# Performance work log

Hardware: AMD Instinct MI355X
Metric: run time of the kernel (lower is better)

## Reference

```python
import math
import jax, jax.numpy as jnp
import numpy as np

DIM = 3
NB = 8  # 2**DIM blades, grade-sorted: [1, e1, e2, e3, e12, e13, e23, e123]
GRADE_SLICES = [(0, 1), (1, 4), (4, 7), (7, 8)]
SUBSPACES = [1, 3, 3, 1]
GRADE_IDX = np.repeat(np.arange(4), SUBSPACES)  # blade -> grade index
EPS = 1e-6
SQRT2 = math.sqrt(2.0)


def _build_cayley():
    # Cl(3,0) Euclidean Cayley table, blades sorted by (grade, bitmask).
    masks = sorted(range(NB), key=lambda m: (bin(m).count("1"), m))
    pos = {m: i for i, m in enumerate(masks)}
    cay = np.zeros((NB, NB, NB), dtype=np.float32)
    for i, mi in enumerate(masks):
        for k, mk in enumerate(masks):
            a, s = mi >> 1, 0
            while a:
                s += bin(a & mk).count("1")
                a >>= 1
            cay[i, pos[mi ^ mk], k] = -1.0 if (s & 1) else 1.0
    triples = []
    for gi in range(4):
        for gj in range(4):
            for gk in range(4):
                (i0, i1), (j0, j1), (k0, k1) = GRADE_SLICES[gi], GRADE_SLICES[gj], GRADE_SLICES[gk]
                if np.any(cay[i0:i1, j0:j1, k0:k1] != 0):
                    triples.append((gi, gj, gk))
    return cay, triples

CAYLEY_NP, TRIPLES = _build_cayley()
NPATHS = len(TRIPLES)  # 20 nonzero grade-triple paths for Cl(3,0)


def mv_linear(x, w, b=None):
    # x: [B,n,8]; w: [m,n,4] (one weight per grade subspace); bias -> scalar blade only.
    w8 = w[..., GRADE_IDX]  # [m,n,8]
    out = jnp.einsum("bni,mni->bmi", x, w8)
    if b is not None:
        out = out.at[..., 0].add(b)
    return out


def grade_q(x):
    # per-grade squared magnitude (Euclidean metric -> all blade signs +1): [B,n,8]->[B,n,4]
    return jnp.stack([jnp.sum(x[..., s:e] ** 2, axis=-1) for s, e in GRADE_SLICES], axis=-1)


def normalization(x, a):
    # CGENN NormalizationLayer (init=0): interpolate per-grade norm toward 1 via sigmoid gate.
    norms = jnp.sqrt(grade_q(x))  # [B,n,4]
    sa = jax.nn.sigmoid(a)  # [n,4]
    norms = sa[None] * (norms - 1.0) + 1.0
    return x / (norms[..., GRADE_IDX] + EPS)


def mv_silu(x, a, b):
    # MVSiLU with invariant='mag2': gate on [scalar, q_grade1, q_grade2, q_grade3].
    q = grade_q(x)  # [B,n,4]
    inv = jnp.concatenate([x[..., :1], q[..., 1:]], axis=-1)  # [B,n,4]
    gate = a[None] * inv + b[None]
    return jax.nn.sigmoid(gate[..., GRADE_IDX]) * x


def fc_geometric_product(x, xr, w, cayley):
    # out[b,m,j] = sum_{n,i,k} x[b,n,i] * cayley[i,j,k] * W[m,n,path(gi,gj,gk)] * xr[b,n,k]
    B, n = x.shape[0], x.shape[1]
    m = w.shape[0]
    out = jnp.zeros((B, m, NB), dtype=x.dtype)
    for t, (gi, gj, gk) in enumerate(TRIPLES):
        (i0, i1), (j0, j1), (k0, k1) = GRADE_SLICES[gi], GRADE_SLICES[gj], GRADE_SLICES[gk]
        tmp = jnp.einsum("bni,ijk,bnk->bnj", x[..., i0:i1], cayley[i0:i1, j0:j1, k0:k1], xr[..., k0:k1])
        out = out.at[:, :, j0:j1].add(jnp.einsum("bnj,mn->bmj", tmp, w[:, :, t]))
    return out


def cw_geometric_product(x, xr, w, cayley):
    # channel-wise steerable GP: out[b,n,j] = sum_{i,k} x[b,n,i]*cayley[i,j,k]*w[n,path]*xr[b,n,k]
    out = jnp.zeros_like(x)
    for t, (gi, gj, gk) in enumerate(TRIPLES):
        (i0, i1), (j0, j1), (k0, k1) = GRADE_SLICES[gi], GRADE_SLICES[gj], GRADE_SLICES[gk]
        tmp = jnp.einsum("bni,ijk,bnk->bnj", x[..., i0:i1], cayley[i0:i1, j0:j1, k0:k1], xr[..., k0:k1])
        out = out.at[:, :, j0:j1].add(tmp * w[None, :, t, None])
    return out


B, IN, HID, OUT = 1024, 256, 512, 128


def setup_inputs():
    key = jax.random.key(0)
    ks = jax.random.split(key, 16)

    def nrm(k, shape, std):
        return jax.random.normal(k, shape, dtype=jnp.float32) * std

    s_in = 1.0 / math.sqrt(IN)
    s_hid = 1.0 / math.sqrt(HID)
    return {
        "x": jax.random.normal(ks[0], (B, IN, NB), dtype=jnp.float32),
        "lr1_w": nrm(ks[1], (IN, IN, 4), s_in),
        "n1_a": jnp.zeros((IN, 4), jnp.float32),
        "ll1_w": nrm(ks[2], (HID, IN, 4), s_in),
        "ll1_b": jnp.zeros((HID,), jnp.float32),
        "w1": nrm(ks[3], (HID, IN, NPATHS), 1.0 / math.sqrt(IN * (DIM + 1))),
        "act_a": jnp.ones((HID, 4), jnp.float32),
        "act_b": jnp.zeros((HID, 4), jnp.float32),
        "lrg_w": nrm(ks[4], (HID, HID, 4), s_hid),
        "ng_a": jnp.zeros((HID, 4), jnp.float32),
        "llg_w": nrm(ks[5], (HID, HID, 4), s_hid),
        "llg_b": jnp.zeros((HID,), jnp.float32),
        "wg": nrm(ks[6], (HID, NPATHS), 1.0 / math.sqrt(DIM + 1)),
        "lr2_w": nrm(ks[7], (HID, HID, 4), s_hid),
        "n2_a": jnp.zeros((HID, 4), jnp.float32),
        "ll2_w": nrm(ks[8], (OUT, HID, 4), s_hid),
        "ll2_b": jnp.zeros((OUT,), jnp.float32),
        "w2": nrm(ks[9], (OUT, HID, NPATHS), 1.0 / math.sqrt(HID * (DIM + 1))),
    }


def reference(x, lr1_w, n1_a, ll1_w, ll1_b, w1, act_a, act_b,
              lrg_w, ng_a, llg_w, llg_b, wg,
              lr2_w, n2_a, ll2_w, ll2_b, w2):
    cayley = jnp.asarray(CAYLEY_NP)
    # fcgp1: right linear -> normalize -> weighted geometric product + first-order term
    xr = normalization(mv_linear(x, lr1_w), n1_a)
    h = (mv_linear(x, ll1_w, ll1_b) + fc_geometric_product(x, xr, w1, cayley)) / SQRT2
    h = mv_silu(h, act_a, act_b)
    # channel-wise steerable geometric product layer
    hr = normalization(mv_linear(h, lrg_w), ng_a)
    h = (mv_linear(h, llg_w, llg_b) + cw_geometric_product(h, hr, wg, cayley)) / SQRT2
    h = mv_silu(h, act_a, act_b)
    # fcgp2
    hr = normalization(mv_linear(h, lr2_w), n2_a)
    out = (mv_linear(h, ll2_w, ll2_b) + fc_geometric_product(h, hr, w2, cayley)) / SQRT2
    return out
```

## Files before the change

kernel.cpp:

```cpp
#include <hip/hip_runtime.h>
#include <math.h>


typedef unsigned short u16;
typedef __attribute__((ext_vector_type(8))) short short8;
typedef __attribute__((ext_vector_type(4))) float f32x4;

#define RSQRT2F 0.70710678118654752440f

__device__ inline void gl_lds16(const void* g, void* l) {
  __builtin_amdgcn_global_load_lds(
      (const __attribute__((address_space(1))) void*)g,
      (__attribute__((address_space(3))) void*)l, 16, 0, 0);
}

__device__ constexpr int PP_I[64] = {
  0,0,0,0,0,0,0,0,  1,1,1,1,1,1,1,1,  2,2,2,2,2,2,2,2,  3,3,3,3,3,3,3,3,
  4,4,4,4,4,4,4,4,  5,5,5,5,5,5,5,5,  6,6,6,6,6,6,6,6,  7,7,7,7,7,7,7,7};
__device__ constexpr int PP_K[64] = {
  0,1,2,3,4,5,6,7,  0,1,2,3,4,5,6,7,  0,1,2,3,4,5,6,7,  0,1,2,3,4,5,6,7,
  0,1,2,3,4,5,6,7,  0,1,2,3,4,5,6,7,  0,1,2,3,4,5,6,7,  0,1,2,3,4,5,6,7};
__device__ constexpr int PP_C[64] = {
   0, 1, 2, 3, 4, 5, 6, 7,
   9, 8,15,16,13,14,21,20,
  10,15, 8,17,12,21,14,19,
  11,16,17, 8,21,12,13,18,
  29,24,23,35,22,34,33,28,
  30,25,35,23,34,22,32,27,
  31,35,25,24,33,32,22,26,
  43,42,41,40,39,38,37,36};
__device__ constexpr int PP_T[64] = {
   0, 1, 1, 1, 2, 2, 2, 3,
   5, 4, 7, 7, 6, 6, 9, 8,
   5, 7, 4, 7, 6, 9, 6, 8,
   5, 7, 7, 4, 9, 6, 6, 8,
  13,11,11,15,10,14,14,12,
  13,11,15,11,14,10,14,12,
  13,15,11,11,14,14,10,12,
  19,18,18,18,17,17,17,16};
__device__ constexpr int PP_J[64] = {
  0,1,2,3,4,5,6,7,
  1,0,4,5,2,3,7,6,
  2,4,0,6,1,7,3,5,
  3,5,6,0,7,1,2,4,
  4,2,1,7,0,6,5,3,
  5,3,7,1,6,0,4,2,
  6,7,3,2,5,4,0,1,
  7,6,5,4,3,2,1,0};
__device__ constexpr float PP_S[64] = {
  1, 1, 1, 1, 1, 1, 1, 1,
  1, 1, 1, 1, 1, 1, 1, 1,
  1,-1, 1, 1,-1,-1, 1,-1,
  1,-1,-1, 1, 1,-1,-1, 1,
  1,-1, 1, 1,-1,-1, 1,-1,
  1,-1,-1, 1, 1,-1,-1, 1,
  1, 1,-1, 1,-1, 1,-1,-1,
  1, 1,-1, 1,-1, 1,-1,-1};

__device__ constexpr int GJ_CNT[8] = {4,6,6,6,6,6,6,4};
__device__ constexpr int GJ_C[8][6] = {
  {0,8,22,36,0,0},
  {1,9,12,23,26,37},
  {2,10,13,24,27,38},
  {3,11,14,25,28,39},
  {4,15,18,29,32,40},
  {5,16,19,30,33,41},
  {6,17,20,31,34,42},
  {7,21,35,43,0,0}};
__device__ constexpr int GJ_T[8][6] = {
  {0,4,10,16,0,0},
  {1,5,6,11,12,17},
  {1,5,6,11,12,17},
  {1,5,6,11,12,17},
  {2,7,8,13,14,18},
  {2,7,8,13,14,18},
  {2,7,8,13,14,18},
  {3,9,15,19,0,0}};
__device__ constexpr int GRADE[8] = {0,1,1,1,2,2,2,3};

__device__ inline float sigm(float x) { return 1.0f / (1.0f + expf(-x)); }
__device__ inline u16 f2bf(float f) {
  unsigned u = __float_as_uint(f);
  return (u16)((u + 0x7fffu + ((u >> 16) & 1u)) >> 16);
}
__device__ inline float bf2f(u16 h) { return __uint_as_float(((unsigned)h) << 16); }

#define BT 128
#define MT 128
#define BKc 64

__global__ __launch_bounds__(256) void mfma_gemm(
    const u16* __restrict__ Alin, const u16* __restrict__ Pfeat,
    const u16* __restrict__ WLin, const u16* __restrict__ WLin2,
    const u16* __restrict__ WGp,
    float* __restrict__ out1, float* __restrict__ out2,
    int N, int M, int aug, int planeA, int planeO, int KSbits, int KCbits)
{
  const int zz    = blockIdx.z;
  const int set   = zz >> (3 + KSbits);
  const int rem   = zz & ((8 << KSbits) - 1);
  const int j     = rem >> KSbits;
  const int slice = rem & ((1 << KSbits) - 1);
  const u16* WL   = set ? WLin2 : WLin;
  float* outp     = set ? out2 : out1;

  const int b0   = blockIdx.y * BT;
  const int m0   = blockIdx.x * MT;
  const int tid  = threadIdx.x;
  const int lane = tid & 63;
  const int wave = tid >> 6;
  const int wr   = wave >> 1;
  const int wc   = wave & 1;
  const int l15  = lane & 15;
  const int lq   = lane >> 4;

  __shared__ u16 As[BT * BKc];
  __shared__ u16 Bs[MT * BKc];

  f32x4 zero = {0.f, 0.f, 0.f, 0.f};
  f32x4 acc[4][4];
  #pragma unroll
  for (int r = 0; r < 4; ++r)
    #pragma unroll
    for (int c = 0; c < 4; ++c) acc[r][c] = zero;

  const int g = GRADE[j];
  const int npass = aug ? (1 + GJ_CNT[j]) : 1;
  const int KC = 1 << KCbits;
  const int cper = (npass << KCbits) >> KSbits;
  const int cbeg = slice * cper;

  const int srow = lane >> 3;
  const int sslot = lane & 7;

  for (int ci = cbeg; ci < cbeg + cper; ++ci) {
    const int p  = ci >> KCbits;
    const int k0 = (ci & (KC - 1)) << 6;
    const u16* Abase = (p == 0) ? Alin + (size_t)j * planeA
                                : Pfeat + (size_t)GJ_C[j][p - 1] * planeA;
    const u16* Wbase = (p == 0) ? WL + (size_t)g * M * N
                                : WGp + (size_t)GJ_T[j][p - 1] * M * N;
    const u16* Asrc = Abase + (size_t)b0 * N + k0;
    const u16* Bsrc = Wbase + (size_t)m0 * N + k0;

    __syncthreads();
    #pragma unroll
    for (int q = 0; q < 4; ++q) {
      int inst = wave * 4 + q;
      int row  = inst * 8 + srow;
      int kg   = sslot ^ (row & 7);
      gl_lds16(Asrc + (size_t)row * N + kg * 8, &As[inst * 512]);
    }
    #pragma unroll
    for (int q = 0; q < 4; ++q) {
      int inst = wave * 4 + q;
      int row  = inst * 8 + srow;
      int kg   = sslot ^ (row & 7);
      gl_lds16(Bsrc + (size_t)row * N + kg * 8, &Bs[inst * 512]);
    }
    __syncthreads();

    #pragma unroll
    for (int s = 0; s < 2; ++s) {
      const int kq = s * 4 + lq;
      short8 af[4], bfr[4];
      #pragma unroll
      for (int r = 0; r < 4; ++r) {
        int row = wr * 64 + r * 16 + l15;
        af[r] = *(const short8*)(&As[row * BKc + (kq ^ (row & 7)) * 8]);
      }
      #pragma unroll
      for (int c = 0; c < 4; ++c) {
        int row = wc * 64 + c * 16 + l15;
        bfr[c] = *(const short8*)(&Bs[row * BKc + (kq ^ (row & 7)) * 8]);
      }
      #pragma unroll
      for (int r = 0; r < 4; ++r)
        #pragma unroll
        for (int c = 0; c < 4; ++c)
          acc[r][c] = __builtin_amdgcn_mfma_f32_16x16x32_bf16(af[r], bfr[c], acc[r][c], 0, 0, 0);
    }
  }

  float* obase = outp + (size_t)(slice * 8 + j) * planeO;
  #pragma unroll
  for (int r = 0; r < 4; ++r)
    #pragma unroll
    for (int c = 0; c < 4; ++c)
      #pragma unroll
      for (int e = 0; e < 4; ++e) {
        int bb = b0 + wr * 64 + r * 16 + lq * 4 + e;
        int mm = m0 + wc * 64 + c * 16 + l15;
        obase[(size_t)bb * M + mm] = acc[r][c][e];
      }
}

struct RepackDesc { const float* in; u16* out; int MN; int S; };
struct RepackArgs { RepackDesc d[8]; const float* x; u16* xp; int PS; };

__global__ void repack_all(RepackArgs a)
{
  int mn = blockIdx.x * 256 + threadIdx.x;
  if (blockIdx.y == 8) {
    if (mn >= a.PS) return;
    float v[8];
    *(float4*)(v)     = *(const float4*)(a.x + (size_t)mn * 8);
    *(float4*)(v + 4) = *(const float4*)(a.x + (size_t)mn * 8 + 4);
    #pragma unroll
    for (int jj = 0; jj < 8; ++jj) a.xp[(size_t)jj * a.PS + mn] = f2bf(v[jj]);
    return;
  }
  RepackDesc d = a.d[blockIdx.y];
  if (mn >= d.MN) return;
  if (d.S == 4) {
    float4 v = ((const float4*)d.in)[mn];
    d.out[(size_t)0 * d.MN + mn] = f2bf(v.x);
    d.out[(size_t)1 * d.MN + mn] = f2bf(v.y);
    d.out[(size_t)2 * d.MN + mn] = f2bf(v.z);
    d.out[(size_t)3 * d.MN + mn] = f2bf(v.w);
  } else {
    #pragma unroll
    for (int q = 0; q < 5; ++q) {
      float4 v = *(const float4*)(d.in + (size_t)mn * 20 + q * 4);
      d.out[(size_t)(q * 4 + 0) * d.MN + mn] = f2bf(v.x);
      d.out[(size_t)(q * 4 + 1) * d.MN + mn] = f2bf(v.y);
      d.out[(size_t)(q * 4 + 2) * d.MN + mn] = f2bf(v.z);
      d.out[(size_t)(q * 4 + 3) * d.MN + mn] = f2bf(v.w);
    }
  }
}

__global__ void pair_norm_p(const u16* __restrict__ up, const float* __restrict__ vpart,
                            const float* __restrict__ na, u16* __restrict__ Pp,
                            int PS, int M, int KS)
{
  int t = blockIdx.x * 256 + threadIdx.x;
  if (t >= PS) return;
  int m = t % M;
  float u[8], v[8];
  #pragma unroll
  for (int jj = 0; jj < 8; ++jj) {
    u[jj] = bf2f(up[(size_t)jj * PS + t]);
    float s = 0.f;
    for (int sl = 0; sl < KS; ++sl) s += vpart[(size_t)(sl * 8 + jj) * PS + t];
    v[jj] = s;
  }
  float q[4];
  q[0] = sqrtf(v[0] * v[0]);
  q[1] = sqrtf(v[1] * v[1] + v[2] * v[2] + v[3] * v[3]);
  q[2] = sqrtf(v[4] * v[4] + v[5] * v[5] + v[6] * v[6]);
  q[3] = sqrtf(v[7] * v[7]);
  float sc[4];
  #pragma unroll
  for (int gg = 0; gg < 4; ++gg) {
    float sa = sigm(na[m * 4 + gg]);
    sc[gg] = 1.0f / (sa * (q[gg] - 1.0f) + 1.0f + 1e-6f);
  }
  #pragma unroll
  for (int jj = 0; jj < 8; ++jj) v[jj] *= sc[GRADE[jj]];
  float p[44];
  #pragma unroll
  for (int c = 0; c < 44; ++c) p[c] = 0.f;
  #pragma unroll
  for (int e = 0; e < 64; ++e)
    p[PP_C[e]] += PP_S[e] * u[PP_I[e]] * v[PP_K[e]];
  #pragma unroll
  for (int c = 0; c < 44; ++c) Pp[(size_t)c * PS + t] = f2bf(p[c]);
}

__global__ void bias_silu_p(const float* __restrict__ hpart, const float* __restrict__ bias,
                            const float* __restrict__ ga, const float* __restrict__ gb,
                            u16* __restrict__ sh, int PS, int M, int KS)
{
  int t = blockIdx.x * 256 + threadIdx.x;
  if (t >= PS) return;
  int m = t % M;
  float v[8];
  #pragma unroll
  for (int jj = 0; jj < 8; ++jj) {
    float s = 0.f;
    for (int sl = 0; sl < KS; ++sl) s += hpart[(size_t)(sl * 8 + jj) * PS + t];
    v[jj] = s;
  }
  v[0] += bias[m];
  #pragma unroll
  for (int jj = 0; jj < 8; ++jj) v[jj] *= RSQRT2F;
  float inv[4];
  inv[0] = v[0];
  inv[1] = v[1]*v[1] + v[2]*v[2] + v[3]*v[3];
  inv[2] = v[4]*v[4] + v[5]*v[5] + v[6]*v[6];
  inv[3] = v[7]*v[7];
  float gt[4];
  #pragma unroll
  for (int gg = 0; gg < 4; ++gg)
    gt[gg] = sigm(ga[m * 4 + gg] * inv[gg] + gb[m * 4 + gg]);
  #pragma unroll
  for (int jj = 0; jj < 8; ++jj)
    sh[(size_t)jj * PS + t] = f2bf(v[jj] * gt[GRADE[jj]]);
}

__global__ void cw_silu_p(const float* __restrict__ llg, const u16* __restrict__ up,
                          const float* __restrict__ hrraw, const float* __restrict__ na,
                          const float* __restrict__ wg, const float* __restrict__ bias,
                          const float* __restrict__ ga, const float* __restrict__ gb,
                          u16* __restrict__ sh, int PS, int M)
{
  int t = blockIdx.x * 256 + threadIdx.x;
  if (t >= PS) return;
  int n = t % M;
  float acc[8], u[8], v[8], w[20];
  #pragma unroll
  for (int jj = 0; jj < 8; ++jj) {
    acc[jj] = llg[(size_t)jj * PS + t];
    u[jj]   = bf2f(up[(size_t)jj * PS + t]);
    v[jj]   = hrraw[(size_t)jj * PS + t];
  }
  float q[4];
  q[0] = sqrtf(v[0] * v[0]);
  q[1] = sqrtf(v[1] * v[1] + v[2] * v[2] + v[3] * v[3]);
  q[2] = sqrtf(v[4] * v[4] + v[5] * v[5] + v[6] * v[6]);
  q[3] = sqrtf(v[7] * v[7]);
  float sc[4];
  #pragma unroll
  for (int gg = 0; gg < 4; ++gg) {
    float sa = sigm(na[n * 4 + gg]);
    sc[gg] = 1.0f / (sa * (q[gg] - 1.0f) + 1.0f + 1e-6f);
  }
  #pragma unroll
  for (int jj = 0; jj < 8; ++jj) v[jj] *= sc[GRADE[jj]];
  #pragma unroll
  for (int qq = 0; qq < 5; ++qq)
    *(float4*)(w + qq * 4) = *(const float4*)(wg + (size_t)n * 20 + qq * 4);
  acc[0] += bias[n];
  #pragma unroll
  for (int e = 0; e < 64; ++e)
    acc[PP_J[e]] += PP_S[e] * u[PP_I[e]] * v[PP_K[e]] * w[PP_T[e]];
  #pragma unroll
  for (int jj = 0; jj < 8; ++jj) acc[jj] *= RSQRT2F;
  float inv[4];
  inv[0] = acc[0];
  inv[1] = acc[1]*acc[1] + acc[2]*acc[2] + acc[3]*acc[3];
  inv[2] = acc[4]*acc[4] + acc[5]*acc[5] + acc[6]*acc[6];
  inv[3] = acc[7]*acc[7];
  float gt[4];
  #pragma unroll
  for (int gg = 0; gg < 4; ++gg)
    gt[gg] = sigm(ga[n * 4 + gg] * inv[gg] + gb[n * 4 + gg]);
  #pragma unroll
  for (int jj = 0; jj < 8; ++jj)
    sh[(size_t)jj * PS + t] = f2bf(acc[jj] * gt[GRADE[jj]]);
}

__global__ void final_p(const float* __restrict__ pre, const float* __restrict__ bias,
                        float* __restrict__ outp, int PS, int M, int KS)
{
  int t = blockIdx.x * 256 + threadIdx.x;
  if (t >= PS) return;
  int m = t % M;
  float v[8];
  #pragma unroll
  for (int jj = 0; jj < 8; ++jj) {
    float s = 0.f;
    for (int sl = 0; sl < KS; ++sl) s += pre[(size_t)(sl * 8 + jj) * PS + t];
    v[jj] = s;
  }
  v[0] += bias[m];
  #pragma unroll
  for (int jj = 0; jj < 8; ++jj) v[jj] *= RSQRT2F;
  *(float4*)(outp + (size_t)t * 8)     = *(float4*)(v);
  *(float4*)(outp + (size_t)t * 8 + 4) = *(float4*)(v + 4);
}

extern "C" void kernel_launch(void* const* d_in, const int* in_sizes, int n_in,
                              void* d_out, int out_size, void* d_ws, size_t ws_size,
                              hipStream_t stream)
{
  const float* x     = (const float*)d_in[0];
  const float* lr1_w = (const float*)d_in[1];
  const float* n1_a  = (const float*)d_in[2];
  const float* ll1_w = (const float*)d_in[3];
  const float* ll1_b = (const float*)d_in[4];
  const float* w1    = (const float*)d_in[5];
  const float* act_a = (const float*)d_in[6];
  const float* act_b = (const float*)d_in[7];
  const float* lrg_w = (const float*)d_in[8];
  const float* ng_a  = (const float*)d_in[9];
  const float* llg_w = (const float*)d_in[10];
  const float* llg_b = (const float*)d_in[11];
  const float* wg    = (const float*)d_in[12];
  const float* lr2_w = (const float*)d_in[13];
  const float* n2_a  = (const float*)d_in[14];
  const float* ll2_w = (const float*)d_in[15];
  const float* ll2_b = (const float*)d_in[16];
  const float* w2    = (const float*)d_in[17];
  float* out = (float*)d_out;

  u16* W = (u16*)d_ws;
  size_t o = 0;
  u16* WL1  = W + o; o +=  262144;
  u16* WLL1 = W + o; o +=  524288;
  u16* WG1  = W + o; o += 2621440;
  u16* WLRG = W + o; o += 1048576;
  u16* WLLG = W + o; o += 1048576;
  u16* WLR2 = W + o; o += 1048576;
  u16* WLL2 = W + o; o +=  262144;
  u16* WG2  = W + o; o += 1310720;
  u16* XB   = W + o; o += 2097152;
  u16* HB   = W + o; o += 4194304;
  u16* P    = W + o; o += 23068672;
  float* f1 = (float*)(W + o);
  float* f2 = f1 + 8388608;
  float* hrP  = f2;
  float* llgP = f2 + 4194304;

  dim3 blk(256);
  const int PS1 = 1024 * 256, PS2 = 1024 * 512, PSO = 1024 * 128;

  RepackArgs ra = {{
    {lr1_w, WL1, 65536, 4}, {ll1_w, WLL1, 131072, 4}, {w1, WG1, 131072, 20},
    {lrg_w, WLRG, 262144, 4}, {llg_w, WLLG, 262144, 4}, {lr2_w, WLR2, 262144, 4},
    {ll2_w, WLL2, 65536, 4}, {w2, WG2, 65536, 20}},
    x, XB, PS1};
  repack_all<<<dim3(1024, 9), blk, 0, stream>>>(ra);

  mfma_gemm<<<dim3(2, 8, 16), blk, 0, stream>>>(XB, nullptr, WL1, nullptr, nullptr,
      f1, nullptr, 256, 256, 0, PS1, PS1, 1, 2);
  pair_norm_p<<<PS1 / 256, blk, 0, stream>>>(XB, f1, n1_a, P, PS1, 256, 2);
  mfma_gemm<<<dim3(4, 8, 16), blk, 0, stream>>>(XB, P, WLL1, nullptr, WG1,
      f1, nullptr, 256, 512, 1, PS1, PS2, 1, 2);
  bias_silu_p<<<PS2 / 256, blk, 0, stream>>>(f1, ll1_b, act_a, act_b, HB, PS2, 512, 2);

  mfma_gemm<<<dim3(4, 8, 16), blk, 0, stream>>>(HB, nullptr, WLRG, WLLG, nullptr,
      hrP, llgP, 512, 512, 0, PS2, PS2, 0, 3);
  cw_silu_p<<<PS2 / 256, blk, 0, stream>>>(llgP, HB, hrP, ng_a, wg, llg_b, act_a, act_b,
      HB, PS2, 512);

  mfma_gemm<<<dim3(4, 8, 16), blk, 0, stream>>>(HB, nullptr, WLR2, nullptr, nullptr,
      f1, nullptr, 512, 512, 0, PS2, PS2, 1, 3);
  pair_norm_p<<<PS2 / 256, blk, 0, stream>>>(HB, f1, n2_a, P, PS2, 512, 2);
  mfma_gemm<<<dim3(1, 8, 64), blk, 0, stream>>>(HB, P, WLL2, nullptr, WG2,
      f1, nullptr, 512, 128, 1, PS2, PSO, 3, 3);
  final_p<<<PSO / 256, blk, 0, stream>>>(f1, ll2_b, out, PSO, 128, 8);
}
```

Baseline: 261.8 us.

## Fuse all stages into one persistent kernel with grid barriers and bf16 intermediates

Replaces the ten separate launches with a single persistent 256-block kernel that loops over GEMM tiles and elementwise work and uses a software grid-wide atomic barrier between stages. GEMM LDS loads are double-buffered with explicit waitcnt so the next k-chunk loads overlap the current MFMAs. Most intermediate GEMM outputs are now stored in bf16 instead of fp32, and split-K is removed in several GEMMs. This cuts launch overhead and intermediate memory traffic. The costs are lower precision, fewer parallel tiles in some stages, and a grid barrier that hangs if not all 256 blocks are co-resident.

```diff
diff --git a/kernel.cpp b/kernel.cpp
--- a/kernel.cpp
+++ b/kernel.cpp
@@ -7,6 +7,10 @@
 typedef __attribute__((ext_vector_type(4))) float f32x4;
 
 #define RSQRT2F 0.70710678118654752440f
+#define NBLK 256
+#define PS1C (1024 * 256)
+#define PS2C (1024 * 512)
+#define PSOC (1024 * 128)
 
 __device__ inline void gl_lds16(const void* g, void* l) {
   __builtin_amdgcn_global_load_lds(
@@ -85,27 +89,83 @@
 }
 __device__ inline float bf2f(u16 h) { return __uint_as_float(((unsigned)h) << 16); }
 
-#define BT 128
-#define MT 128
-#define BKc 64
-
-__global__ __launch_bounds__(256) void mfma_gemm(
+__device__ void gsync(int* bar, int phase) {
+  __syncthreads();
+  if (threadIdx.x == 0) {
+    __threadfence();
+    if (__hip_atomic_fetch_add(&bar[0], 1, __ATOMIC_ACQ_REL,
+                               __HIP_MEMORY_SCOPE_AGENT) == NBLK - 1) {
+      __hip_atomic_store(&bar[0], 0, __ATOMIC_RELAXED, __HIP_MEMORY_SCOPE_AGENT);
+      __hip_atomic_store(&bar[1], phase, __ATOMIC_RELEASE, __HIP_MEMORY_SCOPE_AGENT);
+    } else {
+      while (__hip_atomic_load(&bar[1], __ATOMIC_ACQUIRE,
+                               __HIP_MEMORY_SCOPE_AGENT) < phase)
+        __builtin_amdgcn_s_sleep(8);
+    }
+    __threadfence();
+  }
+  __syncthreads();
+}
+
+struct KArgs {
+  const float* rin[8]; u16* rout[8]; int rMN[8]; int rS[8];
+  const float* x; u16* XB;
+  const float *n1_a, *ll1_b, *act_a, *act_b, *ng_a, *llg_b, *wg, *n2_a, *ll2_b;
+  u16 *WL1, *WLL1, *WG1, *WLRG, *WLLG, *WLR2, *WLL2, *WG2;
+  u16 *HB, *P, *PB16, *hr16, *llg16;
+  float* f1;
+  float* out;
+  int* bar;
+};
+
+__device__ void repack_stage(const KArgs& a) {
+  const int base = blockIdx.x * 256 + threadIdx.x;
+  #pragma unroll 1
+  for (int sec = 0; sec < 8; ++sec) {
+    const float* in = a.rin[sec];
+    u16* outp = a.rout[sec];
+    const int MN = a.rMN[sec];
+    if (a.rS[sec] == 4) {
+      for (int mn = base; mn < MN; mn += NBLK * 256) {
+        float4 v = ((const float4*)in)[mn];
+        outp[(size_t)0 * MN + mn] = f2bf(v.x);
+        outp[(size_t)1 * MN + mn] = f2bf(v.y);
+        outp[(size_t)2 * MN + mn] = f2bf(v.z);
+        outp[(size_t)3 * MN + mn] = f2bf(v.w);
+      }
+    } else {
+      for (int mn = base; mn < MN; mn += NBLK * 256) {
+        #pragma unroll
+        for (int q = 0; q < 5; ++q) {
+          float4 v = *(const float4*)(in + (size_t)mn * 20 + q * 4);
+          outp[(size_t)(q * 4 + 0) * MN + mn] = f2bf(v.x);
+          outp[(size_t)(q * 4 + 1) * MN + mn] = f2bf(v.y);
+          outp[(size_t)(q * 4 + 2) * MN + mn] = f2bf(v.z);
+          outp[(size_t)(q * 4 + 3) * MN + mn] = f2bf(v.w);
+        }
+      }
+    }
+  }
+  for (int mn = base; mn < PS1C; mn += NBLK * 256) {
+    float v[8];
+    *(float4*)(v)     = *(const float4*)(a.x + (size_t)mn * 8);
+    *(float4*)(v + 4) = *(const float4*)(a.x + (size_t)mn * 8 + 4);
+    #pragma unroll
+    for (int jj = 0; jj < 8; ++jj) a.XB[(size_t)jj * PS1C + mn] = f2bf(v[jj]);
+  }
+}
+
+__device__ void gemm_stage(
     const u16* __restrict__ Alin, const u16* __restrict__ Pfeat,
     const u16* __restrict__ WLin, const u16* __restrict__ WLin2,
     const u16* __restrict__ WGp,
-    float* __restrict__ out1, float* __restrict__ out2,
-    int N, int M, int aug, int planeA, int planeO, int KSbits, int KCbits)
+    void* __restrict__ out1, void* __restrict__ out2,
+    int N, int M, int aug, int planeA, int planeO,
+    int KSbits, int KCbits, int out16)
 {
-  const int zz    = blockIdx.z;
-  const int set   = zz >> (3 + KSbits);
-  const int rem   = zz & ((8 << KSbits) - 1);
-  const int j     = rem >> KSbits;
-  const int slice = rem & ((1 << KSbits) - 1);
-  const u16* WL   = set ? WLin2 : WLin;
-  float* outp     = set ? out2 : out1;
-
-  const int b0   = blockIdx.y * BT;
-  const int m0   = blockIdx.x * MT;
+  __shared__ u16 AsB[2][8192];
+  __shared__ u16 BsB[2][8192];
+
   const int tid  = threadIdx.x;
   const int lane = tid & 63;
   const int wave = tid >> 6;
@@ -113,262 +173,285 @@
   const int wc   = wave & 1;
   const int l15  = lane & 15;
   const int lq   = lane >> 4;
-
-  __shared__ u16 As[BT * BKc];
-  __shared__ u16 Bs[MT * BKc];
-
-  f32x4 zero = {0.f, 0.f, 0.f, 0.f};
-  f32x4 acc[4][4];
-  #pragma unroll
-  for (int r = 0; r < 4; ++r)
-    #pragma unroll
-    for (int c = 0; c < 4; ++c) acc[r][c] = zero;
-
-  const int g = GRADE[j];
-  const int npass = aug ? (1 + GJ_CNT[j]) : 1;
-  const int KC = 1 << KCbits;
-  const int cper = (npass << KCbits) >> KSbits;
-  const int cbeg = slice * cper;
-
-  const int srow = lane >> 3;
+  const int srow  = lane >> 3;
   const int sslot = lane & 7;
 
-  for (int ci = cbeg; ci < cbeg + cper; ++ci) {
-    const int p  = ci >> KCbits;
-    const int k0 = (ci & (KC - 1)) << 6;
-    const u16* Abase = (p == 0) ? Alin + (size_t)j * planeA
-                                : Pfeat + (size_t)GJ_C[j][p - 1] * planeA;
-    const u16* Wbase = (p == 0) ? WL + (size_t)g * M * N
-                                : WGp + (size_t)GJ_T[j][p - 1] * M * N;
-    const u16* Asrc = Abase + (size_t)b0 * N + k0;
-    const u16* Bsrc = Wbase + (size_t)m0 * N + k0;
-
-    __syncthreads();
-    #pragma unroll
-    for (int q = 0; q < 4; ++q) {
-      int inst = wave * 4 + q;
-      int row  = inst * 8 + srow;
-      int kg   = sslot ^ (row & 7);
-      gl_lds16(Asrc + (size_t)row * N + kg * 8, &As[inst * 512]);
-    }
-    #pragma unroll
-    for (int q = 0; q < 4; ++q) {
-      int inst = wave * 4 + q;
-      int row  = inst * 8 + srow;
-      int kg   = sslot ^ (row & 7);
-      gl_lds16(Bsrc + (size_t)row * N + kg * 8, &Bs[inst * 512]);
-    }
-    __syncthreads();
-
-    #pragma unroll
-    for (int s = 0; s < 2; ++s) {
-      const int kq = s * 4 + lq;
-      short8 af[4], bfr[4];
+  const int NMX = M >> 7;
+  const int nsets = WLin2 ? 2 : 1;
+  const int KS = 1 << KSbits, KC = 1 << KCbits;
+  const int ntiles = nsets * 8 * KS * 8 * NMX;
+
+  #pragma unroll 1
+  for (int t = blockIdx.x; t < ntiles; t += NBLK) {
+    int tmp = t;
+    const int mx = tmp % NMX; tmp /= NMX;
+    const int by = tmp & 7; tmp >>= 3;
+    const int slice = tmp & (KS - 1); tmp >>= KSbits;
+    const int j = tmp & 7;
+    const int set = tmp >> 3;
+    const u16* WL = set ? WLin2 : WLin;
+    void* outp = set ? out2 : out1;
+    const int b0 = by * 128, m0 = mx * 128;
+    const int g = GRADE[j];
+    const int npass = aug ? (1 + GJ_CNT[j]) : 1;
+    const int cper = (npass << KCbits) >> KSbits;
+    const int cbeg = slice * cper;
+
+    f32x4 acc[4][4];
+    #pragma unroll
+    for (int r = 0; r < 4; ++r)
       #pragma unroll
-      for (int r = 0; r < 4; ++r) {
-        int row = wr * 64 + r * 16 + l15;
-        af[r] = *(const short8*)(&As[row * BKc + (kq ^ (row & 7)) * 8]);
+      for (int c = 0; c < 4; ++c) acc[r][c] = {0.f, 0.f, 0.f, 0.f};
+
+    {
+      const int ci = cbeg;
+      const int p = ci >> KCbits, k0 = (ci & (KC - 1)) << 6;
+      const u16* Ab = (p == 0) ? Alin + (size_t)j * planeA
+                               : Pfeat + (size_t)GJ_C[j][p - 1] * planeA;
+      const u16* Wb = (p == 0) ? WL + (size_t)g * M * N
+                               : WGp + (size_t)GJ_T[j][p - 1] * (size_t)M * N;
+      const u16* As0 = Ab + (size_t)b0 * N + k0;
+      const u16* Bs0 = Wb + (size_t)m0 * N + k0;
+      #pragma unroll
+      for (int q = 0; q < 4; ++q) {
+        int inst = wave * 4 + q, row = inst * 8 + srow;
+        int kg = sslot ^ (row & 7);
+        gl_lds16(As0 + (size_t)row * N + kg * 8, &AsB[0][inst * 512]);
       }
       #pragma unroll
-      for (int c = 0; c < 4; ++c) {
-        int row = wc * 64 + c * 16 + l15;
-        bfr[c] = *(const short8*)(&Bs[row * BKc + (kq ^ (row & 7)) * 8]);
+      for (int q = 0; q < 4; ++q) {
+        int inst = wave * 4 + q, row = inst * 8 + srow;
+        int kg = sslot ^ (row & 7);
+        gl_lds16(Bs0 + (size_t)row * N + kg * 8, &BsB[0][inst * 512]);
       }
+    }
+
+    #pragma unroll 1
+    for (int ci = cbeg; ci < cbeg + cper; ++ci) {
+      const int buf = (ci - cbeg) & 1;
+      if (ci + 1 < cbeg + cper) {
+        const int cn = ci + 1;
+        const int p = cn >> KCbits, k0 = (cn & (KC - 1)) << 6;
+        const u16* Ab = (p == 0) ? Alin + (size_t)j * planeA
+                                 : Pfeat + (size_t)GJ_C[j][p - 1] * planeA;
+        const u16* Wb = (p == 0) ? WL + (size_t)g * M * N
+                                 : WGp + (size_t)GJ_T[j][p - 1] * (size_t)M * N;
+        const u16* As1 = Ab + (size_t)b0 * N + k0;
+        const u16* Bs1 = Wb + (size_t)m0 * N + k0;
+        #pragma unroll
+        for (int q = 0; q < 4; ++q) {
+          int inst = wave * 4 + q, row = inst * 8 + srow;
+          int kg = sslot ^ (row & 7);
+          gl_lds16(As1 + (size_t)row * N + kg * 8, &AsB[1 - buf][inst * 512]);
+        }
+        #pragma unroll
+        for (int q = 0; q < 4; ++q) {
+          int inst = wave * 4 + q, row = inst * 8 + srow;
+          int kg = sslot ^ (row & 7);
+          gl_lds16(Bs1 + (size_t)row * N + kg * 8, &BsB[1 - buf][inst * 512]);
+        }
+        asm volatile("s_waitcnt vmcnt(8)\n\ts_barrier" ::: "memory");
+      } else {
+        asm volatile("s_waitcnt vmcnt(0)\n\ts_barrier" ::: "memory");
+      }
+
+      const u16* As = &AsB[buf][0];
+      const u16* Bs = &BsB[buf][0];
       #pragma unroll
-      for (int r = 0; r < 4; ++r)
-        #pragma unroll
-        for (int c = 0; c < 4; ++c)
-          acc[r][c] = __builtin_amdgcn_mfma_f32_16x16x32_bf16(af[r], bfr[c], acc[r][c], 0, 0, 0);
-    }
-  }
-
-  float* obase = outp + (size_t)(slice * 8 + j) * planeO;
-  #pragma unroll
-  for (int r = 0; r < 4; ++r)
-    #pragma unroll
-    for (int c = 0; c < 4; ++c)
+      for (int s = 0; s < 2; ++s) {
+        const int kq = s * 4 + lq;
+        short8 af[4], bfr[4];
+        #pragma unroll
+        for (int r = 0; r < 4; ++r) {
+          int row = wr * 64 + r * 16 + l15;
+          af[r] = *(const short8*)(&As[row * 64 + (kq ^ (row & 7)) * 8]);
+        }
+        #pragma unroll
+        for (int c = 0; c < 4; ++c) {
+          int row = wc * 64 + c * 16 + l15;
+          bfr[c] = *(const short8*)(&Bs[row * 64 + (kq ^ (row & 7)) * 8]);
+        }
+        #pragma unroll
+        for (int r = 0; r < 4; ++r)
+          #pragma unroll
+          for (int c = 0; c < 4; ++c)
+            acc[r][c] = __builtin_amdgcn_mfma_f32_16x16x32_bf16(af[r], bfr[c], acc[r][c], 0, 0, 0);
+      }
+      asm volatile("s_barrier" ::: "memory");
+    }
+
+    const size_t po = (size_t)(slice * 8 + j) * planeO;
+    #pragma unroll
+    for (int r = 0; r < 4; ++r)
       #pragma unroll
-      for (int e = 0; e < 4; ++e) {
-        int bb = b0 + wr * 64 + r * 16 + lq * 4 + e;
-        int mm = m0 + wc * 64 + c * 16 + l15;
-        obase[(size_t)bb * M + mm] = acc[r][c][e];
-      }
-}
-
-struct RepackDesc { const float* in; u16* out; int MN; int S; };
-struct RepackArgs { RepackDesc d[8]; const float* x; u16* xp; int PS; };
-
-__global__ void repack_all(RepackArgs a)
-{
-  int mn = blockIdx.x * 256 + threadIdx.x;
-  if (blockIdx.y == 8) {
-    if (mn >= a.PS) return;
+      for (int c = 0; c < 4; ++c)
+        #pragma unroll
+        for (int e = 0; e < 4; ++e) {
+          int bb = b0 + wr * 64 + r * 16 + lq * 4 + e;
+          int mm = m0 + wc * 64 + c * 16 + l15;
+          if (out16) ((u16*)outp)[po + (size_t)bb * M + mm] = f2bf(acc[r][c][e]);
+          else       ((float*)outp)[po + (size_t)bb * M + mm] = acc[r][c][e];
+        }
+  }
+}
+
+__device__ void pair_norm_stage(const u16* up, const u16* vpart, const float* na,
+                                u16* Pp, int PS, int M, int KSl) {
+  for (int t = blockIdx.x * 256 + threadIdx.x; t < PS; t += NBLK * 256) {
+    int m = t % M;
+    float u[8], v[8];
+    #pragma unroll
+    for (int jj = 0; jj < 8; ++jj) {
+      u[jj] = bf2f(up[(size_t)jj * PS + t]);
+      float s = 0.f;
+      for (int sl = 0; sl < KSl; ++sl) s += bf2f(vpart[(size_t)(sl * 8 + jj) * PS + t]);
+      v[jj] = s;
+    }
+    float q[4];
+    q[0] = sqrtf(v[0] * v[0]);
+    q[1] = sqrtf(v[1] * v[1] + v[2] * v[2] + v[3] * v[3]);
+    q[2] = sqrtf(v[4] * v[4] + v[5] * v[5] + v[6] * v[6]);
+    q[3] = sqrtf(v[7] * v[7]);
+    float sc[4];
+    #pragma unroll
+    for (int gg = 0; gg < 4; ++gg) {
+      float sa = sigm(na[m * 4 + gg]);
+      sc[gg] = 1.0f / (sa * (q[gg] - 1.0f) + 1.0f + 1e-6f);
+    }
+    #pragma unroll
+    for (int jj = 0; jj < 8; ++jj) v[jj] *= sc[GRADE[jj]];
+    float p[44];
+    #pragma unroll
+    for (int c = 0; c < 44; ++c) p[c] = 0.f;
+    #pragma unroll
+    for (int e = 0; e < 64; ++e)
+      p[PP_C[e]] += PP_S[e] * u[PP_I[e]] * v[PP_K[e]];
+    #pragma unroll
+    for (int c = 0; c < 44; ++c) Pp[(size_t)c * PS + t] = f2bf(p[c]);
+  }
+}
+
+__device__ void bias_silu_stage(const u16* hpre, const float* bias, const float* ga,
+                                const float* gb, u16* sh, int PS, int M) {
+  for (int t = blockIdx.x * 256 + threadIdx.x; t < PS; t += NBLK * 256) {
+    int m = t % M;
     float v[8];
-    *(float4*)(v)     = *(const float4*)(a.x + (size_t)mn * 8);
-    *(float4*)(v + 4) = *(const float4*)(a.x + (size_t)mn * 8 + 4);
-    #pragma unroll
-    for (int jj = 0; jj < 8; ++jj) a.xp[(size_t)jj * a.PS + mn] = f2bf(v[jj]);
-    return;
-  }
-  RepackDesc d = a.d[blockIdx.y];
-  if (mn >= d.MN) return;
-  if (d.S == 4) {
-    float4 v = ((const float4*)d.in)[mn];
-    d.out[(size_t)0 * d.MN + mn] = f2bf(v.x);
-    d.out[(size_t)1 * d.MN + mn] = f2bf(v.y);
-    d.out[(size_t)2 * d.MN + mn] = f2bf(v.z);
-    d.out[(size_t)3 * d.MN + mn] = f2bf(v.w);
-  } else {
-    #pragma unroll
-    for (int q = 0; q < 5; ++q) {
-      float4 v = *(const float4*)(d.in + (size_t)mn * 20 + q * 4);
-      d.out[(size_t)(q * 4 + 0) * d.MN + mn] = f2bf(v.x);
-      d.out[(size_t)(q * 4 + 1) * d.MN + mn] = f2bf(v.y);
-      d.out[(size_t)(q * 4 + 2) * d.MN + mn] = f2bf(v.z);
-      d.out[(size_t)(q * 4 + 3) * d.MN + mn] = f2bf(v.w);
-    }
-  }
-}
-
-__global__ void pair_norm_p(const u16* __restrict__ up, const float* __restrict__ vpart,
-                            const float* __restrict__ na, u16* __restrict__ Pp,
-                            int PS, int M, int KS)
-{
-  int t = blockIdx.x * 256 + threadIdx.x;
-  if (t >= PS) return;
-  int m = t % M;
-  float u[8], v[8];
-  #pragma unroll
-  for (int jj = 0; jj < 8; ++jj) {
-    u[jj] = bf2f(up[(size_t)jj * PS + t]);
-    float s = 0.f;
-    for (int sl = 0; sl < KS; ++sl) s += vpart[(size_t)(sl * 8 + jj) * PS + t];
-    v[jj] = s;
-  }
-  float q[4];
-  q[0] = sqrtf(v[0] * v[0]);
-  q[1] = sqrtf(v[1] * v[1] + v[2] * v[2] + v[3] * v[3]);
-  q[2] = sqrtf(v[4] * v[4] + v[5] * v[5] + v[6] * v[6]);
-  q[3] = sqrtf(v[7] * v[7]);
-  float sc[4];
-  #pragma unroll
-  for (int gg = 0; gg < 4; ++gg) {
-    float sa = sigm(na[m * 4 + gg]);
-    sc[gg] = 1.0f / (sa * (q[gg] - 1.0f) + 1.0f + 1e-6f);
-  }
-  #pragma unroll
-  for (int jj = 0; jj < 8; ++jj) v[jj] *= sc[GRADE[jj]];
-  float p[44];
-  #pragma unroll
-  for (int c = 0; c < 44; ++c) p[c] = 0.f;
-  #pragma unroll
-  for (int e = 0; e < 64; ++e)
-    p[PP_C[e]] += PP_S[e] * u[PP_I[e]] * v[PP_K[e]];
-  #pragma unroll
-  for (int c = 0; c < 44; ++c) Pp[(size_t)c * PS + t] = f2bf(p[c]);
-}
-
-__global__ void bias_silu_p(const float* __restrict__ hpart, const float* __restrict__ bias,
-                            const float* __restrict__ ga, const float* __restrict__ gb,
-                            u16* __restrict__ sh, int PS, int M, int KS)
-{
-  int t = blockIdx.x * 256 + threadIdx.x;
-  if (t >= PS) return;
-  int m = t % M;
-  float v[8];
-  #pragma unroll
-  for (int jj = 0; jj < 8; ++jj) {
-    float s = 0.f;
-    for (int sl = 0; sl < KS; ++sl) s += hpart[(size_t)(sl * 8 + jj) * PS + t];
-    v[jj] = s;
-  }
-  v[0] += bias[m];
-  #pragma unroll
-  for (int jj = 0; jj < 8; ++jj) v[jj] *= RSQRT2F;
-  float inv[4];
-  inv[0] = v[0];
-  inv[1] = v[1]*v[1] + v[2]*v[2] + v[3]*v[3];
-  inv[2] = v[4]*v[4] + v[5]*v[5] + v[6]*v[6];
-  inv[3] = v[7]*v[7];
-  float gt[4];
-  #pragma unroll
-  for (int gg = 0; gg < 4; ++gg)
-    gt[gg] = sigm(ga[m * 4 + gg] * inv[gg] + gb[m * 4 + gg]);
-  #pragma unroll
-  for (int jj = 0; jj < 8; ++jj)
-    sh[(size_t)jj * PS + t] = f2bf(v[jj] * gt[GRADE[jj]]);
-}
-
-__global__ void cw_silu_p(const float* __restrict__ llg, const u16* __restrict__ up,
-                          const float* __restrict__ hrraw, const float* __restrict__ na,
-                          const float* __restrict__ wg, const float* __restrict__ bias,
-                          const float* __restrict__ ga, const float* __restrict__ gb,
-                          u16* __restrict__ sh, int PS, int M)
-{
-  int t = blockIdx.x * 256 + threadIdx.x;
-  if (t >= PS) return;
-  int n = t % M;
-  float acc[8], u[8], v[8], w[20];
-  #pragma unroll
-  for (int jj = 0; jj < 8; ++jj) {
-    acc[jj] = llg[(size_t)jj * PS + t];
-    u[jj]   = bf2f(up[(size_t)jj * PS + t]);
-    v[jj]   = hrraw[(size_t)jj * PS + t];
-  }
-  float q[4];
-  q[0] = sqrtf(v[0] * v[0]);
-  q[1] = sqrtf(v[1] * v[1] + v[2] * v[2] + v[3] * v[3]);
-  q[2] = sqrtf(v[4] * v[4] + v[5] * v[5] + v[6] * v[6]);
-  q[3] = sqrtf(v[7] * v[7]);
-  float sc[4];
-  #pragma unroll
-  for (int gg = 0; gg < 4; ++gg) {
-    float sa = sigm(na[n * 4 + gg]);
-    sc[gg] = 1.0f / (sa * (q[gg] - 1.0f) + 1.0f + 1e-6f);
-  }
-  #pragma unroll
-  for (int jj = 0; jj < 8; ++jj) v[jj] *= sc[GRADE[jj]];
-  #pragma unroll
-  for (int qq = 0; qq < 5; ++qq)
-    *(float4*)(w + qq * 4) = *(const float4*)(wg + (size_t)n * 20 + qq * 4);
-  acc[0] += bias[n];
-  #pragma unroll
-  for (int e = 0; e < 64; ++e)
-    acc[PP_J[e]] += PP_S[e] * u[PP_I[e]] * v[PP_K[e]] * w[PP_T[e]];
-  #pragma unroll
-  for (int jj = 0; jj < 8; ++jj) acc[jj] *= RSQRT2F;
-  float inv[4];
-  inv[0] = acc[0];
-  inv[1] = acc[1]*acc[1] + acc[2]*acc[2] + acc[3]*acc[3];
-  inv[2] = acc[4]*acc[4] + acc[5]*acc[5] + acc[6]*acc[6];
-  inv[3] = acc[7]*acc[7];
-  float gt[4];
-  #pragma unroll
-  for (int gg = 0; gg < 4; ++gg)
-    gt[gg] = sigm(ga[n * 4 + gg] * inv[gg] + gb[n * 4 + gg]);
-  #pragma unroll
-  for (int jj = 0; jj < 8; ++jj)
-    sh[(size_t)jj * PS + t] = f2bf(acc[jj] * gt[GRADE[jj]]);
-}
-
-__global__ void final_p(const float* __restrict__ pre, const float* __restrict__ bias,
-                        float* __restrict__ outp, int PS, int M, int KS)
-{
-  int t = blockIdx.x * 256 + threadIdx.x;
-  if (t >= PS) return;
-  int m = t % M;
-  float v[8];
-  #pragma unroll
-  for (int jj = 0; jj < 8; ++jj) {
-    float s = 0.f;
-    for (int sl = 0; sl < KS; ++sl) s += pre[(size_t)(sl * 8 + jj) * PS + t];
-    v[jj] = s;
-  }
-  v[0] += bias[m];
-  #pragma unroll
-  for (int jj = 0; jj < 8; ++jj) v[jj] *= RSQRT2F;
-  *(float4*)(outp + (size_t)t * 8)     = *(float4*)(v);
-  *(float4*)(outp + (size_t)t * 8 + 4) = *(float4*)(v + 4);
+    #pragma unroll
+    for (int jj = 0; jj < 8; ++jj) v[jj] = bf2f(hpre[(size_t)jj * PS + t]);
+    v[0] += bias[m];
+    #pragma unroll
+    for (int jj = 0; jj < 8; ++jj) v[jj] *= RSQRT2F;
+    float inv[4];
+    inv[0] = v[0];
+    inv[1] = v[1]*v[1] + v[2]*v[2] + v[3]*v[3];
+    inv[2] = v[4]*v[4] + v[5]*v[5] + v[6]*v[6];
+    inv[3] = v[7]*v[7];
+    float gt[4];
+    #pragma unroll
+    for (int gg = 0; gg < 4; ++gg)
+      gt[gg] = sigm(ga[m * 4 + gg] * inv[gg] + gb[m * 4 + gg]);
+    #pragma unroll
+    for (int jj = 0; jj < 8; ++jj)
+      sh[(size_t)jj * PS + t] = f2bf(v[jj] * gt[GRADE[jj]]);
+  }
+}
+
+__device__ void cw_silu_stage(const u16* llg, const u16* up, const u16* hrraw,
+                              const float* na, const float* wg, const float* bias,
+                              const float* ga, const float* gb, u16* sh, int PS, int M) {
+  for (int t = blockIdx.x * 256 + threadIdx.x; t < PS; t += NBLK * 256) {
+    int n = t % M;
+    float acc[8], u[8], v[8], w[20];
+    #pragma unroll
+    for (int jj = 0; jj < 8; ++jj) {
+      acc[jj] = bf2f(llg[(size_t)jj * PS + t]);
+      u[jj]   = bf2f(up[(size_t)jj * PS + t]);
+      v[jj]   = bf2f(hrraw[(size_t)jj * PS + t]);
+    }
+    float q[4];
+    q[0] = sqrtf(v[0] * v[0]);
+    q[1] = sqrtf(v[1] * v[1] + v[2] * v[2] + v[3] * v[3]);
+    q[2] = sqrtf(v[4] * v[4] + v[5] * v[5] + v[6] * v[6]);
+    q[3] = sqrtf(v[7] * v[7]);
+    float sc[4];
+    #pragma unroll
+    for (int gg = 0; gg < 4; ++gg) {
+      float sa = sigm(na[n * 4 + gg]);
+      sc[gg] = 1.0f / (sa * (q[gg] - 1.0f) + 1.0f + 1e-6f);
+    }
+    #pragma unroll
+    for (int jj = 0; jj < 8; ++jj) v[jj] *= sc[GRADE[jj]];
+    #pragma unroll
+    for (int qq = 0; qq < 5; ++qq)
+      *(float4*)(w + qq * 4) = *(const float4*)(wg + (size_t)n * 20 + qq * 4);
+    acc[0] += bias[n];
+    #pragma unroll
+    for (int e = 0; e < 64; ++e)
+      acc[PP_J[e]] += PP_S[e] * u[PP_I[e]] * v[PP_K[e]] * w[PP_T[e]];
+    #pragma unroll
+    for (int jj = 0; jj < 8; ++jj) acc[jj] *= RSQRT2F;
+    float inv[4];
+    inv[0] = acc[0];
+    inv[1] = acc[1]*acc[1] + acc[2]*acc[2] + acc[3]*acc[3];
+    inv[2] = acc[4]*acc[4] + acc[5]*acc[5] + acc[6]*acc[6];
+    inv[3] = acc[7]*acc[7];
+    float gt[4];
+    #pragma unroll
+    for (int gg = 0; gg < 4; ++gg)
+      gt[gg] = sigm(ga[n * 4 + gg] * inv[gg] + gb[n * 4 + gg]);
+    #pragma unroll
+    for (int jj = 0; jj < 8; ++jj)
+      sh[(size_t)jj * PS + t] = f2bf(acc[jj] * gt[GRADE[jj]]);
+  }
+}
+
+__device__ void final_stage(const float* pre, const float* bias, float* outp,
+                            int PS, int M, int KSl) {
+  for (int t = blockIdx.x * 256 + threadIdx.x; t < PS; t += NBLK * 256) {
+    int m = t % M;
+    float v[8];
+    #pragma unroll
+    for (int jj = 0; jj < 8; ++jj) {
+      float s = 0.f;
+      for (int sl = 0; sl < KSl; ++sl) s += pre[(size_t)(sl * 8 + jj) * PS + t];
+      v[jj] = s;
+    }
+    v[0] += bias[m];
+    #pragma unroll
+    for (int jj = 0; jj < 8; ++jj) v[jj] *= RSQRT2F;
+    *(float4*)(outp + (size_t)t * 8)     = *(float4*)(v);
+    *(float4*)(outp + (size_t)t * 8 + 4) = *(float4*)(v + 4);
+  }
+}
+
+__global__ __launch_bounds__(256, 1) void mega(KArgs a) {
+  repack_stage(a);
+  gsync(a.bar, 1);
+  gemm_stage(a.XB, nullptr, a.WL1, nullptr, nullptr, a.PB16, nullptr,
+             256, 256, 0, PS1C, PS1C, 1, 2, 1);
+  gsync(a.bar, 2);
+  pair_norm_stage(a.XB, a.PB16, a.n1_a, a.P, PS1C, 256, 2);
+  gsync(a.bar, 3);
+  gemm_stage(a.XB, a.P, a.WLL1, nullptr, a.WG1, a.PB16, nullptr,
+             256, 512, 1, PS1C, PS2C, 0, 2, 1);
+  gsync(a.bar, 4);
+  bias_silu_stage(a.PB16, a.ll1_b, a.act_a, a.act_b, a.HB, PS2C, 512);
+  gsync(a.bar, 5);
+  gemm_stage(a.HB, nullptr, a.WLRG, a.WLLG, nullptr, a.hr16, a.llg16,
+             512, 512, 0, PS2C, PS2C, 0, 3, 1);
+  gsync(a.bar, 6);
+  cw_silu_stage(a.llg16, a.HB, a.hr16, a.ng_a, a.wg, a.llg_b, a.act_a, a.act_b,
+                a.HB, PS2C, 512);
+  gsync(a.bar, 7);
+  gemm_stage(a.HB, nullptr, a.WLR2, nullptr, nullptr, a.PB16, nullptr,
+             512, 512, 0, PS2C, PS2C, 0, 3, 1);
+  gsync(a.bar, 8);
+  pair_norm_stage(a.HB, a.PB16, a.n2_a, a.P, PS2C, 512, 1);
+  gsync(a.bar, 9);
+  gemm_stage(a.HB, a.P, a.WLL2, nullptr, a.WG2, a.f1, nullptr,
+             512, 128, 1, PS2C, PSOC, 3, 3, 0);
+  gsync(a.bar, 10);
+  final_stage(a.f1, a.ll2_b, a.out, PSOC, 128, 8);
 }
 
 extern "C" void kernel_launch(void* const* d_in, const int* in_sizes, int n_in,
@@ -393,7 +476,6 @@
   const float* ll2_w = (const float*)d_in[15];
   const float* ll2_b = (const float*)d_in[16];
   const float* w2    = (const float*)d_in[17];
-  float* out = (float*)d_out;
 
   u16* W = (u16*)d_ws;
   size_t o = 0;
@@ -408,37 +490,27 @@
   u16* XB   = W + o; o += 2097152;
   u16* HB   = W + o; o += 4194304;
   u16* P    = W + o; o += 23068672;
-  float* f1 = (float*)(W + o);
-  float* f2 = f1 + 8388608;
-  float* hrP  = f2;
-  float* llgP = f2 + 4194304;
-
-  dim3 blk(256);
-  const int PS1 = 1024 * 256, PS2 = 1024 * 512, PSO = 1024 * 128;
-
-  RepackArgs ra = {{
-    {lr1_w, WL1, 65536, 4}, {ll1_w, WLL1, 131072, 4}, {w1, WG1, 131072, 20},
-    {lrg_w, WLRG, 262144, 4}, {llg_w, WLLG, 262144, 4}, {lr2_w, WLR2, 262144, 4},
-    {ll2_w, WLL2, 65536, 4}, {w2, WG2, 65536, 20}},
-    x, XB, PS1};
-  repack_all<<<dim3(1024, 9), blk, 0, stream>>>(ra);
-
-  mfma_gemm<<<dim3(2, 8, 16), blk, 0, stream>>>(XB, nullptr, WL1, nullptr, nullptr,
-      f1, nullptr, 256, 256, 0, PS1, PS1, 1, 2);
-  pair_norm_p<<<PS1 / 256, blk, 0, stream>>>(XB, f1, n1_a, P, PS1, 256, 2);
-  mfma_gemm<<<dim3(4, 8, 16), blk, 0, stream>>>(XB, P, WLL1, nullptr, WG1,
-      f1, nullptr, 256, 512, 1, PS1, PS2, 1, 2);
-  bias_silu_p<<<PS2 / 256, blk, 0, stream>>>(f1, ll1_b, act_a, act_b, HB, PS2, 512, 2);
-
-  mfma_gemm<<<dim3(4, 8, 16), blk, 0, stream>>>(HB, nullptr, WLRG, WLLG, nullptr,
-      hrP, llgP, 512, 512, 0, PS2, PS2, 0, 3);
-  cw_silu_p<<<PS2 / 256, blk, 0, stream>>>(llgP, HB, hrP, ng_a, wg, llg_b, act_a, act_b,
-      HB, PS2, 512);
-
-  mfma_gemm<<<dim3(4, 8, 16), blk, 0, stream>>>(HB, nullptr, WLR2, nullptr, nullptr,
-      f1, nullptr, 512, 512, 0, PS2, PS2, 1, 3);
-  pair_norm_p<<<PS2 / 256, blk, 0, stream>>>(HB, f1, n2_a, P, PS2, 512, 2);
-  mfma_gemm<<<dim3(1, 8, 64), blk, 0, stream>>>(HB, P, WLL2, nullptr, WG2,
-      f1, nullptr, 512, 128, 1, PS2, PSO, 3, 3);
-  final_p<<<PSO / 256, blk, 0, stream>>>(f1, ll2_b, out, PSO, 128, 8);
-}
+  u16* PB16 = W + o; o += 8388608;
+  u16* HRG  = W + o; o += 8388608;
+  u16* hr16  = HRG;
+  u16* llg16 = HRG + 4194304;
+  float* f1  = (float*)(W + o);
+  int* bar   = (int*)(f1 + 8388608);
+
+  KArgs a;
+  const float* rins[8] = {lr1_w, ll1_w, w1, lrg_w, llg_w, lr2_w, ll2_w, w2};
+  u16* routs[8] = {WL1, WLL1, WG1, WLRG, WLLG, WLR2, WLL2, WG2};
+  int rmns[8] = {65536, 131072, 131072, 262144, 262144, 262144, 65536, 65536};
+  int rss[8]  = {4, 4, 20, 4, 4, 4, 4, 20};
+  for (int i = 0; i < 8; ++i) { a.rin[i] = rins[i]; a.rout[i] = routs[i]; a.rMN[i] = rmns[i]; a.rS[i] = rss[i]; }
+  a.x = x; a.XB = XB;
+  a.n1_a = n1_a; a.ll1_b = ll1_b; a.act_a = act_a; a.act_b = act_b;
+  a.ng_a = ng_a; a.llg_b = llg_b; a.wg = wg; a.n2_a = n2_a; a.ll2_b = ll2_b;
+  a.WL1 = WL1; a.WLL1 = WLL1; a.WG1 = WG1; a.WLRG = WLRG; a.WLLG = WLLG;
+  a.WLR2 = WLR2; a.WLL2 = WLL2; a.WG2 = WG2;
+  a.HB = HB; a.P = P; a.PB16 = PB16; a.hr16 = hr16; a.llg16 = llg16;
+  a.f1 = f1; a.out = (float*)d_out; a.bar = bar;
+
+  hipMemsetAsync(bar, 0, 16, stream);
+  mega<<<NBLK, 256, 0, stream>>>(a);
+}
```

Result: slower. 648.2 us (+147.6%).
